# Kernel tuning notes

Hardware: AMD Instinct MI355X
Metric: run time of the kernel (lower is better)

## Reference

```python
import jax, jax.numpy as jnp
import numpy as np

N = 100000    # nodes
E = 800000    # directed edges
EF = 16       # edge features
NF = 1        # node features (forced by the module's MLP-size constraint)
HID = NF * 8  # NNConv out = 8
H1, C1 = 8, 16  # gat1 heads / per-head channels -> 128
NC = 16       # num_classes (gat2: heads=1, out=NC)


def setup_inputs() -> dict:
    key = jax.random.key(0)
    ks = jax.random.split(key, 20)
    s = 0.1
    return {
        "x": jax.random.normal(ks[0], (N, NF), jnp.float32),
        "edge_index": jax.random.randint(ks[1], (2, E), 0, N, jnp.int64),
        "edge_attr": jax.random.normal(ks[2], (E, EF), jnp.float32),
        # edge MLP: Linear(EF,8) -> ReLU -> Linear(8,8)
        "w1": jax.random.normal(ks[3], (EF, HID), jnp.float32) * s,
        "b1": jnp.zeros((HID,), jnp.float32),
        "w2": jax.random.normal(ks[4], (HID, HID), jnp.float32) * s,
        "b2": jnp.zeros((HID,), jnp.float32),
        # NNConv root weight + bias
        "root": jax.random.normal(ks[5], (NF, HID), jnp.float32) * s,
        "nn_bias": jnp.zeros((HID,), jnp.float32),
        # GAT1: in 8 -> 16 ch x 8 heads
        "g1W": jax.random.normal(ks[6], (HID, H1 * C1), jnp.float32) * s,
        "g1as": jax.random.normal(ks[7], (H1, C1), jnp.float32) * s,
        "g1ad": jax.random.normal(ks[8], (H1, C1), jnp.float32) * s,
        "g1b": jnp.zeros((H1 * C1,), jnp.float32),
        # GAT2: in 128 -> NC, 1 head
        "g2W": jax.random.normal(ks[9], (H1 * C1, NC), jnp.float32) * s,
        "g2as": jax.random.normal(ks[10], (1, NC), jnp.float32) * s,
        "g2ad": jax.random.normal(ks[11], (1, NC), jnp.float32) * s,
        "g2b": jnp.zeros((NC,), jnp.float32),
    }


def _gat(h_in, W, a_src, a_dst, bias, src, dst, n, heads, ch):
    # h: [N, heads, ch]
    h = (h_in @ W).reshape(n, heads, ch)
    e_s = jnp.einsum("nhc,hc->nh", h, a_src)   # per-node src logits
    e_d = jnp.einsum("nhc,hc->nh", h, a_dst)
    e = jax.nn.leaky_relu(e_s[src] + e_d[dst], 0.2)      # [E2, heads]
    m = jax.ops.segment_max(e, dst, num_segments=n)      # segment softmax
    e = jnp.exp(e - m[dst])
    z = jax.ops.segment_sum(e, dst, num_segments=n)
    alpha = e / (z[dst] + 1e-16)                          # [E2, heads]
    out = jax.ops.segment_sum(alpha[:, :, None] * h[src], dst, num_segments=n)
    return out.reshape(n, heads * ch) + bias


def reference(x, edge_index, edge_attr, w1, b1, w2, b2, root, nn_bias,
              g1W, g1as, g1ad, g1b, g2W, g2as, g2ad, g2b):
    n = x.shape[0]
    src, dst = edge_index[0], edge_index[1]

    # ---- NNConv (aggr='mean'): per-edge weight from edge MLP ----
    w_e = jax.nn.relu(edge_attr @ w1 + b1) @ w2 + b2      # [E, NF*HID]
    w_e = w_e.reshape(-1, NF, HID)
    msg = jnp.einsum("ei,eio->eo", x[src], w_e)            # [E, HID]
    sums = jax.ops.segment_sum(msg, dst, num_segments=n)
    cnt = jax.ops.segment_sum(jnp.ones((msg.shape[0],), msg.dtype), dst, num_segments=n)
    aggr = sums / jnp.maximum(cnt, 1.0)[:, None]
    h = jax.nn.relu(aggr + x @ root + nn_bias)             # [N, 8]
    # dropout: eval mode -> identity

    # ---- add self-loops (PyG GATConv default) ----
    loops = jnp.arange(n, dtype=src.dtype)
    src2 = jnp.concatenate([src, loops])
    dst2 = jnp.concatenate([dst, loops])

    h = jax.nn.elu(_gat(h, g1W, g1as, g1ad, g1b, src2, dst2, n, H1, C1))  # [N,128]
    out = _gat(h, g2W, g2as, g2ad, g2b, src2, dst2, n, 1, NC)             # [N,16]
    return jax.nn.log_softmax(out, axis=1)
```

## Files before the change

### kernel.cpp

```cpp
#include <hip/hip_runtime.h>
#include <hip/hip_fp16.h>
#include <math.h>

constexpr int NN  = 100000;
constexpr int NE  = 800000;
constexpr int H1 = 8, C1 = 16;
constexpr int D1 = H1 * C1;
constexpr int NC = 16;
constexpr int CAP = 40;
constexpr float LOG2E = 1.44269504f;

static inline int cdiv(int a, int b) { return (a + b - 1) / b; }

typedef int   v4i __attribute__((ext_vector_type(4)));
typedef float v2f __attribute__((ext_vector_type(2)));

__device__ inline __half2 h2_bits(unsigned u) {
    __half2 r; __builtin_memcpy(&r, &u, 4); return r;
}
__device__ inline __half2 shflx_h2(__half2 v, int off) {
    int iv; __builtin_memcpy(&iv, &v, 4);
    iv = __shfl_xor(iv, off);
    __half2 r; __builtin_memcpy(&r, &iv, 4); return r;
}

__global__ void fill_cur(int* __restrict__ cur) {
    int i = blockIdx.x * blockDim.x + threadIdx.x;
    if (i < NN) cur[i] = i * CAP;
}

__global__ void nnconv_scatter(const float* __restrict__ x,
                               const int* __restrict__ src, const int* __restrict__ dst,
                               const float* __restrict__ ea,
                               const float* __restrict__ w1, const float* __restrict__ b1,
                               const float* __restrict__ w2, const float* __restrict__ b2,
                               int* __restrict__ cursor,
                               int* __restrict__ src_s, __half* __restrict__ msg_s) {
    __shared__ float sw1[16 * 8], sw2[8 * 8], sb1[8], sb2[8];
    int t = threadIdx.x;
    if (t < 128) sw1[t] = w1[t];
    else if (t < 192) sw2[t - 128] = w2[t - 128];
    else if (t < 200) sb1[t - 192] = b1[t - 192];
    else if (t < 208) sb2[t - 200] = b2[t - 200];
    __syncthreads();
    int e = blockIdx.x * blockDim.x + t;
    if (e >= NE) return;

    float a[16];
    const float4* ea4 = (const float4*)(ea + (size_t)e * 16);
    float4 v0 = ea4[0], v1 = ea4[1], v2 = ea4[2], v3 = ea4[3];
    a[0]=v0.x; a[1]=v0.y; a[2]=v0.z; a[3]=v0.w;
    a[4]=v1.x; a[5]=v1.y; a[6]=v1.z; a[7]=v1.w;
    a[8]=v2.x; a[9]=v2.y; a[10]=v2.z; a[11]=v2.w;
    a[12]=v3.x; a[13]=v3.y; a[14]=v3.z; a[15]=v3.w;

    float hdn[8];
#pragma unroll
    for (int j = 0; j < 8; j++) {
        float s = sb1[j];
#pragma unroll
        for (int i = 0; i < 16; i++) s = fmaf(a[i], sw1[i * 8 + j], s);
        hdn[j] = fmaxf(s, 0.f);
    }
    int sn = src[e], dn = dst[e];
    float xv = x[sn];
    __align__(16) __half msg[8];
#pragma unroll
    for (int j = 0; j < 8; j++) {
        float s = sb2[j];
#pragma unroll
        for (int i = 0; i < 8; i++) s = fmaf(hdn[i], sw2[i * 8 + j], s);
        msg[j] = __float2half(xv * s);
    }
    int pos = atomicAdd(&cursor[dn], 1);
    if (pos < dn * CAP + CAP) {
        v4i mv; __builtin_memcpy(&mv, msg, 16);
        __builtin_nontemporal_store(mv, (v4i*)(msg_s + (unsigned)pos * 8u));
        src_s[pos] = sn;
    }
}

__global__ void fused_node1(const float* __restrict__ x,
                            const int* __restrict__ cur,
                            const __half* __restrict__ msg_s,
                            const float* __restrict__ root, const float* __restrict__ nb,
                            const float* __restrict__ W,
                            const float* __restrict__ as_, const float* __restrict__ ad_,
                            unsigned char* __restrict__ h1f8,
                            float* __restrict__ es, float* __restrict__ ed) {
    int t = blockIdx.x * blockDim.x + threadIdx.x;
    if (t >= NN * 8) return;
    int n = t >> 3, j = t & 7;
    int rs = n * CAP;
    int d = min(cur[n] - rs, CAP);

    float p0 = 0.f, p1 = 0.f, p2 = 0.f, p3 = 0.f;
    float p4 = 0.f, p5 = 0.f, p6 = 0.f, p7 = 0.f;
    for (int k = j; k < d; k += 8) {
        uint4 m = *(const uint4*)(msg_s + (unsigned)(rs + k) * 8u);
        float2 f0 = __half22float2(h2_bits(m.x));
        float2 f1 = __half22float2(h2_bits(m.y));
        float2 f2 = __half22float2(h2_bits(m.z));
        float2 f3 = __half22float2(h2_bits(m.w));
        p0 += f0.x; p1 += f0.y; p2 += f1.x; p3 += f1.y;
        p4 += f2.x; p5 += f2.y; p6 += f3.x; p7 += f3.y;
    }
    float k0 = (j & 4) ? p4 : p0, s0 = (j & 4) ? p0 : p4;
    float k1 = (j & 4) ? p5 : p1, s1 = (j & 4) ? p1 : p5;
    float k2 = (j & 4) ? p6 : p2, s2 = (j & 4) ? p2 : p6;
    float k3 = (j & 4) ? p7 : p3, s3 = (j & 4) ? p3 : p7;
    k0 += __shfl_xor(s0, 4); k1 += __shfl_xor(s1, 4);
    k2 += __shfl_xor(s2, 4); k3 += __shfl_xor(s3, 4);
    float m0 = (j & 2) ? k2 : k0, n0 = (j & 2) ? k0 : k2;
    float m1 = (j & 2) ? k3 : k1, n1 = (j & 2) ? k1 : k3;
    m0 += __shfl_xor(n0, 2); m1 += __shfl_xor(n1, 2);
    float q  = (j & 1) ? m1 : m0, r = (j & 1) ? m0 : m1;
    float sum = q + __shfl_xor(r, 1);

    float hj = fmaxf(sum / fmaxf((float)d, 1.f) + x[n] * root[j] + nb[j], 0.f);

    float hv[8];
#pragma unroll
    for (int k = 0; k < 8; k++) hv[k] = __shfl(hj, k, 8);

    int hd = j;
    float acc[16];
#pragma unroll
    for (int c = 0; c < 16; c++) acc[c] = 0.f;
#pragma unroll
    for (int k = 0; k < 8; k++) {
        const float* wr = W + k * D1 + hd * 16;
#pragma unroll
        for (int c = 0; c < 16; c++) acc[c] = fmaf(hv[k], wr[c], acc[c]);
    }
    float s = 0.f, dd = 0.f;
#pragma unroll
    for (int c = 0; c < 16; c++) {
        s = fmaf(acc[c], as_[hd * 16 + c], s);
        dd = fmaf(acc[c], ad_[hd * 16 + c], dd);
    }
    v4i pk;
#pragma unroll
    for (int w = 0; w < 4; w++) {
        int wd = __builtin_amdgcn_cvt_pk_fp8_f32(acc[4*w] * 16.f, acc[4*w+1] * 16.f, 0, false);
        wd = __builtin_amdgcn_cvt_pk_fp8_f32(acc[4*w+2] * 16.f, acc[4*w+3] * 16.f, wd, true);
        pk[w] = wd;
    }
    *(v4i*)(h1f8 + (unsigned)n * 128u + hd * 16) = pk;
    es[t] = s * LOG2E;
    ed[t] = dd * LOG2E;
}

__global__ __launch_bounds__(256) void gat1_gather(
        const int* __restrict__ cur,
        const int* __restrict__ src_s,
        const float* __restrict__ es, const float* __restrict__ ed,
        const unsigned char* __restrict__ h1f8, const float* __restrict__ b,
        const float* __restrict__ W2,
        const float* __restrict__ as2, const float* __restrict__ ad2,
        __half* __restrict__ h2h, float* __restrict__ es2, float* __restrict__ ed2) {
    __shared__ float sW2[2048];
    __shared__ float so[4][4][132];
    int tid = threadIdx.x;
    for (int idx = tid; idx < 2048; idx += 256) sW2[idx] = W2[idx];
    __syncthreads();

    int wv = tid >> 6, lane = tid & 63;
    int g  = lane >> 4;
    int cl = lane & 15;
    int hd = cl >> 1;
    float4 bv0 = *((const float4*)(b + cl * 8));
    float4 bv1 = *((const float4*)(b + cl * 8 + 4));

    int base = (blockIdx.x * 4 + wv) * 4;
    for (int i = 0; i < 4; i++) {
        int node = base + i;
        int rs = node * CAP;
        int d = min(cur[node] - rs, CAP);
        const int* sp = src_s + rs;
        float edn = ed[(unsigned)node * 8u + hd];

        float vs = es[(unsigned)node * 8u + hd] + edn;
        vs = fmaxf(vs, 0.2f * vs);
        float a0 = (g == 0) ? __builtin_amdgcn_exp2f(vs) : 0.f;
        float z = a0;
        uint2 gl = *(const uint2*)(h1f8 + (unsigned)node * 128u + cl * 8);
        v2f d0 = __builtin_amdgcn_cvt_pk_f32_fp8(gl.x, false);
        v2f d1 = __builtin_amdgcn_cvt_pk_f32_fp8(gl.x, true);
        v2f d2 = __builtin_amdgcn_cvt_pk_f32_fp8(gl.y, false);
        v2f d3 = __builtin_amdgcn_cvt_pk_f32_fp8(gl.y, true);
        float c0 = a0 * d0[0], c1 = a0 * d0[1], c2 = a0 * d1[0], c3 = a0 * d1[1];
        float c4 = a0 * d2[0], c5 = a0 * d2[1], c6 = a0 * d3[0], c7 = a0 * d3[1];

        for (int k = g; k < d; k += 4) {
            int s = sp[k];
            float v = es[(unsigned)s * 8u + hd] + edn;
            v = fmaxf(v, 0.2f * v);
            float a = __builtin_amdgcn_exp2f(v);
            uint2 ge = *(const uint2*)(h1f8 + (unsigned)s * 128u + cl * 8);
            v2f e0 = __builtin_amdgcn_cvt_pk_f32_fp8(ge.x, false);
            v2f e1 = __builtin_amdgcn_cvt_pk_f32_fp8(ge.x, true);
            v2f e2 = __builtin_amdgcn_cvt_pk_f32_fp8(ge.y, false);
            v2f e3 = __builtin_amdgcn_cvt_pk_f32_fp8(ge.y, true);
            z += a;
            c0 = fmaf(a, e0[0], c0); c1 = fmaf(a, e0[1], c1);
            c2 = fmaf(a, e1[0], c2); c3 = fmaf(a, e1[1], c3);
            c4 = fmaf(a, e2[0], c4); c5 = fmaf(a, e2[1], c5);
            c6 = fmaf(a, e3[0], c6); c7 = fmaf(a, e3[1], c7);
        }
        z += __shfl_xor(z, 16); z += __shfl_xor(z, 32);
        c0 += __shfl_xor(c0, 16); c0 += __shfl_xor(c0, 32);
        c1 += __shfl_xor(c1, 16); c1 += __shfl_xor(c1, 32);
        c2 += __shfl_xor(c2, 16); c2 += __shfl_xor(c2, 32);
        c3 += __shfl_xor(c3, 16); c3 += __shfl_xor(c3, 32);
        c4 += __shfl_xor(c4, 16); c4 += __shfl_xor(c4, 32);
        c5 += __shfl_xor(c5, 16); c5 += __shfl_xor(c5, 32);
        c6 += __shfl_xor(c6, 16); c6 += __shfl_xor(c6, 32);
        c7 += __shfl_xor(c7, 16); c7 += __shfl_xor(c7, 32);

        float rz = 1.f / (16.f * (z + 1e-16f));
        float o0 = fmaf(c0, rz, bv0.x), o1 = fmaf(c1, rz, bv0.y);
        float o2 = fmaf(c2, rz, bv0.z), o3 = fmaf(c3, rz, bv0.w);
        float o4 = fmaf(c4, rz, bv1.x), o5 = fmaf(c5, rz, bv1.y);
        float o6 = fmaf(c6, rz, bv1.z), o7 = fmaf(c7, rz, bv1.w);
        o0 = o0 > 0.f ? o0 : __expf(o0) - 1.f;
        o1 = o1 > 0.f ? o1 : __expf(o1) - 1.f;
        o2 = o2 > 0.f ? o2 : __expf(o2) - 1.f;
        o3 = o3 > 0.f ? o3 : __expf(o3) - 1.f;
        o4 = o4 > 0.f ? o4 : __expf(o4) - 1.f;
        o5 = o5 > 0.f ? o5 : __expf(o5) - 1.f;
        o6 = o6 > 0.f ? o6 : __expf(o6) - 1.f;
        o7 = o7 > 0.f ? o7 : __expf(o7) - 1.f;
        if (g == 0) {
            float4* sp2 = (float4*)&so[wv][i][cl * 8];
            sp2[0] = make_float4(o0, o1, o2, o3);
            sp2[1] = make_float4(o4, o5, o6, o7);
        }
    }
    __asm__ __volatile__("s_waitcnt lgkmcnt(0)" ::: "memory");

    int nl = lane >> 4, c = lane & 15;
    float partial = 0.f;
#pragma unroll 4
    for (int k = 0; k < 128; k += 2) {
        float2 sv = *(const float2*)&so[wv][nl][k];
        partial = fmaf(sv.x, sW2[k * 16 + c], partial);
        partial = fmaf(sv.y, sW2[(k + 1) * 16 + c], partial);
    }
    float ta = partial * as2[c], tb = partial * ad2[c];
#pragma unroll
    for (int off = 1; off < 16; off <<= 1) {
        ta += __shfl_xor(ta, off);
        tb += __shfl_xor(tb, off);
    }
    h2h[(unsigned)(base + nl) * 16u + c] = __float2half(partial);
    if (c == 0) {
        es2[base + nl] = ta * LOG2E;
        ed2[base + nl] = tb * LOG2E;
    }
}

__global__ __launch_bounds__(256) void gat2_gather(
        const int* __restrict__ cur,
        const int* __restrict__ src_s,
        const float* __restrict__ es, const float* __restrict__ ed,
        const __half* __restrict__ h2h, const float* __restrict__ b,
        float* __restrict__ out) {
    int tid = threadIdx.x;
    int wv = tid >> 6, lane = tid & 63;
    int g = lane >> 3, l = lane & 7;
    const unsigned* h2i = (const unsigned*)h2h;
    float2 bv = ((const float2*)b)[l];
    int base = (blockIdx.x * 4 + wv) * 4;
    for (int i = 0; i < 4; i++) {
        int node = base + i;
        int rs = node * CAP;
        int d = min(cur[node] - rs, CAP);
        const int* sp = src_s + rs;
        float edn = ed[node];
        float vs = es[node] + edn;
        vs = fmaxf(vs, 0.2f * vs);
        float a0 = (g == 0) ? __builtin_amdgcn_exp2f(vs) : 0.f;
        float z = a0;
        __half2 acc = __hmul2(__float2half2_rn(a0),
                              h2_bits(h2i[(unsigned)node * 8u + l]));

        for (int k = g; k < d; k += 8) {
            int s = sp[k];
            float v = es[s] + edn;
            v = fmaxf(v, 0.2f * v);
            float a = __builtin_amdgcn_exp2f(v);
            unsigned hraw = h2i[(unsigned)s * 8u + l];
            z += a;
            acc = __hfma2(__float2half2_rn(a), h2_bits(hraw), acc);
        }
        z += __shfl_xor(z, 8); z += __shfl_xor(z, 16); z += __shfl_xor(z, 32);
        acc = __hadd2(acc, shflx_h2(acc, 8));
        acc = __hadd2(acc, shflx_h2(acc, 16));
        acc = __hadd2(acc, shflx_h2(acc, 32));

        float rz = 1.f / (z + 1e-16f);
        float2 f = __half22float2(acc);
        float o0 = fmaf(f.x, rz, bv.x);
        float o1 = fmaf(f.y, rz, bv.y);
        float mx = fmaxf(o0, o1);
        mx = fmaxf(mx, __shfl_xor(mx, 1));
        mx = fmaxf(mx, __shfl_xor(mx, 2));
        mx = fmaxf(mx, __shfl_xor(mx, 4));
        float ss = __expf(o0 - mx) + __expf(o1 - mx);
        ss += __shfl_xor(ss, 1); ss += __shfl_xor(ss, 2); ss += __shfl_xor(ss, 4);
        float lg = mx + __logf(ss);
        if (g == 0)
            ((float2*)out)[(unsigned)node * 8u + l] = make_float2(o0 - lg, o1 - lg);
    }
}

extern "C" void kernel_launch(void* const* d_in, const int* in_sizes, int n_in,
                              void* d_out, int out_size, void* d_ws, size_t ws_size,
                              hipStream_t stream) {
    const float* x    = (const float*)d_in[0];
    const int*   ei   = (const int*)d_in[1];
    const float* ea   = (const float*)d_in[2];
    const float* w1   = (const float*)d_in[3];
    const float* b1   = (const float*)d_in[4];
    const float* w2   = (const float*)d_in[5];
    const float* b2   = (const float*)d_in[6];
    const float* root = (const float*)d_in[7];
    const float* nb   = (const float*)d_in[8];
    const float* g1W  = (const float*)d_in[9];
    const float* g1as = (const float*)d_in[10];
    const float* g1ad = (const float*)d_in[11];
    const float* g1b  = (const float*)d_in[12];
    const float* g2W  = (const float*)d_in[13];
    const float* g2as = (const float*)d_in[14];
    const float* g2ad = (const float*)d_in[15];
    const float* g2b  = (const float*)d_in[16];
    float* out = (float*)d_out;

    const int* src = ei;
    const int* dst = ei + NE;

    float* ws = (float*)d_ws;
    size_t o = 0;
    __half* msg_s  = (__half*)(ws + o); o += (size_t)NN * CAP * 4;
    unsigned char* h1f8 = (unsigned char*)(ws + o); o += (size_t)NN * 32;
    __half* h2h    = (__half*)(ws + o); o += (size_t)NN * NC / 2;
    int*  src_s = (int*)(ws + o); o += (size_t)NN * CAP;
    int*  cur   = (int*)(ws + o); o += NN;
    float* es1  = ws + o; o += (size_t)NN * H1;
    float* ed1  = ws + o; o += (size_t)NN * H1;
    float* es2  = ws + o; o += NN;
    float* ed2  = ws + o; o += NN;
    (void)ws_size; (void)in_sizes; (void)n_in; (void)out_size;

    const int B = 256;

    fill_cur<<<cdiv(NN, B), B, 0, stream>>>(cur);

    nnconv_scatter<<<cdiv(NE, B), B, 0, stream>>>(x, src, dst, ea, w1, b1, w2, b2,
                                                  cur, src_s, msg_s);
    fused_node1<<<cdiv(NN * 8, B), B, 0, stream>>>(x, cur, msg_s, root, nb,
                                                   g1W, g1as, g1ad, h1f8, es1, ed1);
    gat1_gather<<<NN / 16, B, 0, stream>>>(cur, src_s, es1, ed1, h1f8,
                                           g1b, g2W, g2as, g2ad, h2h, es2, ed2);
    gat2_gather<<<NN / 16, B, 0, stream>>>(cur, src_s, es2, ed2, h2h, g2b, out);
}
```

Measured before the change: 299.3 us.

## Move edge MLP from scatter into node aggregation, store (src, edge id) slots

The scatter kernel now only builds the per-destination slot list, storing source index and edge id as an int2 and no longer computing or writing fp16 messages. The node kernel reads each slot, gathers the edge attributes by edge id, recomputes the edge MLP message in fp32 and sums it. This removes the msg_s write and reread and the fp16 rounding of messages, but swaps a sequential streaming read of edge_attr for a random 64-byte gather per edge. The GAT kernels now read source indices with stride 2, which uses more bandwidth on those index loads.

```diff
diff --git a/kernel.cpp b/kernel.cpp
--- a/kernel.cpp
+++ b/kernel.cpp
@@ -29,66 +29,38 @@
     if (i < NN) cur[i] = i * CAP;
 }
 
-__global__ void nnconv_scatter(const float* __restrict__ x,
-                               const int* __restrict__ src, const int* __restrict__ dst,
-                               const float* __restrict__ ea,
-                               const float* __restrict__ w1, const float* __restrict__ b1,
-                               const float* __restrict__ w2, const float* __restrict__ b2,
-                               int* __restrict__ cursor,
-                               int* __restrict__ src_s, __half* __restrict__ msg_s) {
-    __shared__ float sw1[16 * 8], sw2[8 * 8], sb1[8], sb2[8];
-    int t = threadIdx.x;
-    if (t < 128) sw1[t] = w1[t];
-    else if (t < 192) sw2[t - 128] = w2[t - 128];
-    else if (t < 200) sb1[t - 192] = b1[t - 192];
-    else if (t < 208) sb2[t - 200] = b2[t - 200];
-    __syncthreads();
-    int e = blockIdx.x * blockDim.x + t;
+__global__ void scatter_csr(const int* __restrict__ src, const int* __restrict__ dst,
+                            int* __restrict__ cursor, int* __restrict__ slots) {
+    int e = blockIdx.x * blockDim.x + threadIdx.x;
     if (e >= NE) return;
-
-    float a[16];
-    const float4* ea4 = (const float4*)(ea + (size_t)e * 16);
-    float4 v0 = ea4[0], v1 = ea4[1], v2 = ea4[2], v3 = ea4[3];
-    a[0]=v0.x; a[1]=v0.y; a[2]=v0.z; a[3]=v0.w;
-    a[4]=v1.x; a[5]=v1.y; a[6]=v1.z; a[7]=v1.w;
-    a[8]=v2.x; a[9]=v2.y; a[10]=v2.z; a[11]=v2.w;
-    a[12]=v3.x; a[13]=v3.y; a[14]=v3.z; a[15]=v3.w;
-
-    float hdn[8];
-#pragma unroll
-    for (int j = 0; j < 8; j++) {
-        float s = sb1[j];
-#pragma unroll
-        for (int i = 0; i < 16; i++) s = fmaf(a[i], sw1[i * 8 + j], s);
-        hdn[j] = fmaxf(s, 0.f);
-    }
     int sn = src[e], dn = dst[e];
-    float xv = x[sn];
-    __align__(16) __half msg[8];
-#pragma unroll
-    for (int j = 0; j < 8; j++) {
-        float s = sb2[j];
-#pragma unroll
-        for (int i = 0; i < 8; i++) s = fmaf(hdn[i], sw2[i * 8 + j], s);
-        msg[j] = __float2half(xv * s);
-    }
     int pos = atomicAdd(&cursor[dn], 1);
     if (pos < dn * CAP + CAP) {
-        v4i mv; __builtin_memcpy(&mv, msg, 16);
-        __builtin_nontemporal_store(mv, (v4i*)(msg_s + (unsigned)pos * 8u));
-        src_s[pos] = sn;
+        int2 v; v.x = sn; v.y = e;
+        *(int2*)(slots + (size_t)pos * 2) = v;
     }
 }
 
 __global__ void fused_node1(const float* __restrict__ x,
                             const int* __restrict__ cur,
-                            const __half* __restrict__ msg_s,
+                            const int* __restrict__ slots,
+                            const float* __restrict__ ea,
+                            const float* __restrict__ w1, const float* __restrict__ b1,
+                            const float* __restrict__ w2, const float* __restrict__ b2,
                             const float* __restrict__ root, const float* __restrict__ nb,
                             const float* __restrict__ W,
                             const float* __restrict__ as_, const float* __restrict__ ad_,
                             unsigned char* __restrict__ h1f8,
                             float* __restrict__ es, float* __restrict__ ed) {
-    int t = blockIdx.x * blockDim.x + threadIdx.x;
+    __shared__ float sw1[16 * 8], sw2[8 * 8], sb1[8], sb2[8];
+    int tl = threadIdx.x;
+    if (tl < 128) sw1[tl] = w1[tl];
+    else if (tl < 192) sw2[tl - 128] = w2[tl - 128];
+    else if (tl < 200) sb1[tl - 192] = b1[tl - 192];
+    else if (tl < 208) sb2[tl - 200] = b2[tl - 200];
+    __syncthreads();
+
+    int t = blockIdx.x * blockDim.x + tl;
     if (t >= NN * 8) return;
     int n = t >> 3, j = t & 7;
     int rs = n * CAP;
@@ -97,13 +69,34 @@
     float p0 = 0.f, p1 = 0.f, p2 = 0.f, p3 = 0.f;
     float p4 = 0.f, p5 = 0.f, p6 = 0.f, p7 = 0.f;
     for (int k = j; k < d; k += 8) {
-        uint4 m = *(const uint4*)(msg_s + (unsigned)(rs + k) * 8u);
-        float2 f0 = __half22float2(h2_bits(m.x));
-        float2 f1 = __half22float2(h2_bits(m.y));
-        float2 f2 = __half22float2(h2_bits(m.z));
-        float2 f3 = __half22float2(h2_bits(m.w));
-        p0 += f0.x; p1 += f0.y; p2 += f1.x; p3 += f1.y;
-        p4 += f2.x; p5 += f2.y; p6 += f3.x; p7 += f3.y;
+        int2 se = *(const int2*)(slots + (size_t)(rs + k) * 2);
+        int sn = se.x, eid = se.y;
+        float xv = x[sn];
+        const float4* ea4 = (const float4*)(ea + (size_t)eid * 16);
+        float4 v0 = ea4[0], v1 = ea4[1], v2 = ea4[2], v3 = ea4[3];
+        float a[16];
+        a[0]=v0.x; a[1]=v0.y; a[2]=v0.z; a[3]=v0.w;
+        a[4]=v1.x; a[5]=v1.y; a[6]=v1.z; a[7]=v1.w;
+        a[8]=v2.x; a[9]=v2.y; a[10]=v2.z; a[11]=v2.w;
+        a[12]=v3.x; a[13]=v3.y; a[14]=v3.z; a[15]=v3.w;
+        float hdn[8];
+#pragma unroll
+        for (int c = 0; c < 8; c++) {
+            float s = sb1[c];
+#pragma unroll
+            for (int i = 0; i < 16; i++) s = fmaf(a[i], sw1[i * 8 + c], s);
+            hdn[c] = fmaxf(s, 0.f);
+        }
+        float m[8];
+#pragma unroll
+        for (int c = 0; c < 8; c++) {
+            float s = sb2[c];
+#pragma unroll
+            for (int i = 0; i < 8; i++) s = fmaf(hdn[i], sw2[i * 8 + c], s);
+            m[c] = xv * s;
+        }
+        p0 += m[0]; p1 += m[1]; p2 += m[2]; p3 += m[3];
+        p4 += m[4]; p5 += m[5]; p6 += m[6]; p7 += m[7];
     }
     float k0 = (j & 4) ? p4 : p0, s0 = (j & 4) ? p0 : p4;
     float k1 = (j & 4) ? p5 : p1, s1 = (j & 4) ? p1 : p5;
@@ -153,7 +146,7 @@
 
 __global__ __launch_bounds__(256) void gat1_gather(
         const int* __restrict__ cur,
-        const int* __restrict__ src_s,
+        const int* __restrict__ slots,
         const float* __restrict__ es, const float* __restrict__ ed,
         const unsigned char* __restrict__ h1f8, const float* __restrict__ b,
         const float* __restrict__ W2,
@@ -177,7 +170,7 @@
         int node = base + i;
         int rs = node * CAP;
         int d = min(cur[node] - rs, CAP);
-        const int* sp = src_s + rs;
+        const int* sp = slots + (size_t)rs * 2;
         float edn = ed[(unsigned)node * 8u + hd];
 
         float vs = es[(unsigned)node * 8u + hd] + edn;
@@ -193,7 +186,7 @@
         float c4 = a0 * d2[0], c5 = a0 * d2[1], c6 = a0 * d3[0], c7 = a0 * d3[1];
 
         for (int k = g; k < d; k += 4) {
-            int s = sp[k];
+            int s = sp[k << 1];
             float v = es[(unsigned)s * 8u + hd] + edn;
             v = fmaxf(v, 0.2f * v);
             float a = __builtin_amdgcn_exp2f(v);
@@ -262,7 +255,7 @@
 
 __global__ __launch_bounds__(256) void gat2_gather(
         const int* __restrict__ cur,
-        const int* __restrict__ src_s,
+        const int* __restrict__ slots,
         const float* __restrict__ es, const float* __restrict__ ed,
         const __half* __restrict__ h2h, const float* __restrict__ b,
         float* __restrict__ out) {
@@ -276,7 +269,7 @@
         int node = base + i;
         int rs = node * CAP;
         int d = min(cur[node] - rs, CAP);
-        const int* sp = src_s + rs;
+        const int* sp = slots + (size_t)rs * 2;
         float edn = ed[node];
         float vs = es[node] + edn;
         vs = fmaxf(vs, 0.2f * vs);
@@ -286,7 +279,7 @@
                               h2_bits(h2i[(unsigned)node * 8u + l]));
 
         for (int k = g; k < d; k += 8) {
-            int s = sp[k];
+            int s = sp[k << 1];
             float v = es[s] + edn;
             v = fmaxf(v, 0.2f * v);
             float a = __builtin_amdgcn_exp2f(v);
@@ -342,10 +335,9 @@
 
     float* ws = (float*)d_ws;
     size_t o = 0;
-    __half* msg_s  = (__half*)(ws + o); o += (size_t)NN * CAP * 4;
+    int* slots = (int*)(ws + o); o += (size_t)NN * CAP * 2;
     unsigned char* h1f8 = (unsigned char*)(ws + o); o += (size_t)NN * 32;
     __half* h2h    = (__half*)(ws + o); o += (size_t)NN * NC / 2;
-    int*  src_s = (int*)(ws + o); o += (size_t)NN * CAP;
     int*  cur   = (int*)(ws + o); o += NN;
     float* es1  = ws + o; o += (size_t)NN * H1;
     float* ed1  = ws + o; o += (size_t)NN * H1;
@@ -357,11 +349,11 @@
 
     fill_cur<<<cdiv(NN, B), B, 0, stream>>>(cur);
 
-    nnconv_scatter<<<cdiv(NE, B), B, 0, stream>>>(x, src, dst, ea, w1, b1, w2, b2,
-                                                  cur, src_s, msg_s);
-    fused_node1<<<cdiv(NN * 8, B), B, 0, stream>>>(x, cur, msg_s, root, nb,
-                                                   g1W, g1as, g1ad, h1f8, es1, ed1);
-    gat1_gather<<<NN / 16, B, 0, stream>>>(cur, src_s, es1, ed1, h1f8,
+    scatter_csr<<<cdiv(NE, B), B, 0, stream>>>(src, dst, cur, slots);
+    fused_node1<<<cdiv(NN * 8, B), B, 0, stream>>>(x, cur, slots, ea, w1, b1, w2, b2,
+                                                   root, nb, g1W, g1as, g1ad,
+                                                   h1f8, es1, ed1);
+    gat1_gather<<<NN / 16, B, 0, stream>>>(cur, slots, es1, ed1, h1f8,
                                            g1b, g2W, g2as, g2ad, h2h, es2, ed2);
-    gat2_gather<<<NN / 16, B, 0, stream>>>(cur, src_s, es2, ed2, h2h, g2b, out);
-}
+    gat2_gather<<<NN / 16, B, 0, stream>>>(cur, slots, es2, ed2, h2h, g2b, out);
+}
```

Measured after the change: 531.9 us. 77.7% more time.

## Pack source index and FP8 NNConv message into one 16-byte edge record

Applied to the files above, without the earlier changes.

The scatter kernel now writes a single interleaved 16-byte record per edge, holding the source index and the eight messages quantized to FP8 with a scale of 32. Before, it wrote a separate half-precision message array plus a separate source-index array. The point is one store per edge instead of two, which cuts the scattered memory transactions in the atomic-placement pass. The cost is that the GAT gather kernels now read source indices at a 16-byte stride, which wastes bandwidth on those reads. FP8 messages also lose precision relative to fp16.

```diff
diff --git a/kernel.cpp b/kernel.cpp
--- a/kernel.cpp
+++ b/kernel.cpp
@@ -9,6 +9,7 @@
 constexpr int NC = 16;
 constexpr int CAP = 40;
 constexpr float LOG2E = 1.44269504f;
+constexpr float MSC   = 32.f;
 
 static inline int cdiv(int a, int b) { return (a + b - 1) / b; }
 
@@ -35,7 +36,7 @@
                                const float* __restrict__ w1, const float* __restrict__ b1,
                                const float* __restrict__ w2, const float* __restrict__ b2,
                                int* __restrict__ cursor,
-                               int* __restrict__ src_s, __half* __restrict__ msg_s) {
+                               int* __restrict__ rec_s) {
     __shared__ float sw1[16 * 8], sw2[8 * 8], sb1[8], sb2[8];
     int t = threadIdx.x;
     if (t < 128) sw1[t] = w1[t];
@@ -63,26 +64,30 @@
         hdn[j] = fmaxf(s, 0.f);
     }
     int sn = src[e], dn = dst[e];
-    float xv = x[sn];
-    __align__(16) __half msg[8];
+    float xv = x[sn] * MSC;
+    float m[8];
 #pragma unroll
     for (int j = 0; j < 8; j++) {
         float s = sb2[j];
 #pragma unroll
         for (int i = 0; i < 8; i++) s = fmaf(hdn[i], sw2[i * 8 + j], s);
-        msg[j] = __float2half(xv * s);
-    }
+        m[j] = xv * s;
+    }
+    int wa = __builtin_amdgcn_cvt_pk_fp8_f32(m[0], m[1], 0, false);
+    wa     = __builtin_amdgcn_cvt_pk_fp8_f32(m[2], m[3], wa, true);
+    int wb = __builtin_amdgcn_cvt_pk_fp8_f32(m[4], m[5], 0, false);
+    wb     = __builtin_amdgcn_cvt_pk_fp8_f32(m[6], m[7], wb, true);
+
     int pos = atomicAdd(&cursor[dn], 1);
     if (pos < dn * CAP + CAP) {
-        v4i mv; __builtin_memcpy(&mv, msg, 16);
-        __builtin_nontemporal_store(mv, (v4i*)(msg_s + (unsigned)pos * 8u));
-        src_s[pos] = sn;
+        v4i rec; rec[0] = sn; rec[1] = wa; rec[2] = wb; rec[3] = 0;
+        __builtin_nontemporal_store(rec, (v4i*)(rec_s + (size_t)pos * 4));
     }
 }
 
 __global__ void fused_node1(const float* __restrict__ x,
                             const int* __restrict__ cur,
-                            const __half* __restrict__ msg_s,
+                            const int* __restrict__ rec_s,
                             const float* __restrict__ root, const float* __restrict__ nb,
                             const float* __restrict__ W,
                             const float* __restrict__ as_, const float* __restrict__ ad_,
@@ -97,13 +102,13 @@
     float p0 = 0.f, p1 = 0.f, p2 = 0.f, p3 = 0.f;
     float p4 = 0.f, p5 = 0.f, p6 = 0.f, p7 = 0.f;
     for (int k = j; k < d; k += 8) {
-        uint4 m = *(const uint4*)(msg_s + (unsigned)(rs + k) * 8u);
-        float2 f0 = __half22float2(h2_bits(m.x));
-        float2 f1 = __half22float2(h2_bits(m.y));
-        float2 f2 = __half22float2(h2_bits(m.z));
-        float2 f3 = __half22float2(h2_bits(m.w));
-        p0 += f0.x; p1 += f0.y; p2 += f1.x; p3 += f1.y;
-        p4 += f2.x; p5 += f2.y; p6 += f3.x; p7 += f3.y;
+        uint4 m = *(const uint4*)(rec_s + (size_t)(rs + k) * 4);
+        v2f f0 = __builtin_amdgcn_cvt_pk_f32_fp8(m.y, false);
+        v2f f1 = __builtin_amdgcn_cvt_pk_f32_fp8(m.y, true);
+        v2f f2 = __builtin_amdgcn_cvt_pk_f32_fp8(m.z, false);
+        v2f f3 = __builtin_amdgcn_cvt_pk_f32_fp8(m.z, true);
+        p0 += f0[0]; p1 += f0[1]; p2 += f1[0]; p3 += f1[1];
+        p4 += f2[0]; p5 += f2[1]; p6 += f3[0]; p7 += f3[1];
     }
     float k0 = (j & 4) ? p4 : p0, s0 = (j & 4) ? p0 : p4;
     float k1 = (j & 4) ? p5 : p1, s1 = (j & 4) ? p1 : p5;
@@ -117,7 +122,8 @@
     float q  = (j & 1) ? m1 : m0, r = (j & 1) ? m0 : m1;
     float sum = q + __shfl_xor(r, 1);
 
-    float hj = fmaxf(sum / fmaxf((float)d, 1.f) + x[n] * root[j] + nb[j], 0.f);
+    float inv = 1.f / (MSC * fmaxf((float)d, 1.f));
+    float hj = fmaxf(fmaf(sum, inv, x[n] * root[j] + nb[j]), 0.f);
 
     float hv[8];
 #pragma unroll
@@ -153,7 +159,7 @@
 
 __global__ __launch_bounds__(256) void gat1_gather(
         const int* __restrict__ cur,
-        const int* __restrict__ src_s,
+        const int* __restrict__ rec_s,
         const float* __restrict__ es, const float* __restrict__ ed,
         const unsigned char* __restrict__ h1f8, const float* __restrict__ b,
         const float* __restrict__ W2,
@@ -177,7 +183,7 @@
         int node = base + i;
         int rs = node * CAP;
         int d = min(cur[node] - rs, CAP);
-        const int* sp = src_s + rs;
+        const int* sp = rec_s + (size_t)rs * 4;
         float edn = ed[(unsigned)node * 8u + hd];
 
         float vs = es[(unsigned)node * 8u + hd] + edn;
@@ -193,7 +199,7 @@
         float c4 = a0 * d2[0], c5 = a0 * d2[1], c6 = a0 * d3[0], c7 = a0 * d3[1];
 
         for (int k = g; k < d; k += 4) {
-            int s = sp[k];
+            int s = sp[k << 2];
             float v = es[(unsigned)s * 8u + hd] + edn;
             v = fmaxf(v, 0.2f * v);
             float a = __builtin_amdgcn_exp2f(v);
@@ -262,7 +268,7 @@
 
 __global__ __launch_bounds__(256) void gat2_gather(
         const int* __restrict__ cur,
-        const int* __restrict__ src_s,
+        const int* __restrict__ rec_s,
         const float* __restrict__ es, const float* __restrict__ ed,
         const __half* __restrict__ h2h, const float* __restrict__ b,
         float* __restrict__ out) {
@@ -276,7 +282,7 @@
         int node = base + i;
         int rs = node * CAP;
         int d = min(cur[node] - rs, CAP);
-        const int* sp = src_s + rs;
+        const int* sp = rec_s + (size_t)rs * 4;
         float edn = ed[node];
         float vs = es[node] + edn;
         vs = fmaxf(vs, 0.2f * vs);
@@ -286,7 +292,7 @@
                               h2_bits(h2i[(unsigned)node * 8u + l]));
 
         for (int k = g; k < d; k += 8) {
-            int s = sp[k];
+            int s = sp[k << 2];
             float v = es[s] + edn;
             v = fmaxf(v, 0.2f * v);
             float a = __builtin_amdgcn_exp2f(v);
@@ -342,10 +348,9 @@
 
     float* ws = (float*)d_ws;
     size_t o = 0;
-    __half* msg_s  = (__half*)(ws + o); o += (size_t)NN * CAP * 4;
+    int* rec_s = (int*)(ws + o); o += (size_t)NN * CAP * 4;
     unsigned char* h1f8 = (unsigned char*)(ws + o); o += (size_t)NN * 32;
     __half* h2h    = (__half*)(ws + o); o += (size_t)NN * NC / 2;
-    int*  src_s = (int*)(ws + o); o += (size_t)NN * CAP;
     int*  cur   = (int*)(ws + o); o += NN;
     float* es1  = ws + o; o += (size_t)NN * H1;
     float* ed1  = ws + o; o += (size_t)NN * H1;
@@ -358,10 +363,10 @@
     fill_cur<<<cdiv(NN, B), B, 0, stream>>>(cur);
 
     nnconv_scatter<<<cdiv(NE, B), B, 0, stream>>>(x, src, dst, ea, w1, b1, w2, b2,
-                                                  cur, src_s, msg_s);
-    fused_node1<<<cdiv(NN * 8, B), B, 0, stream>>>(x, cur, msg_s, root, nb,
+                                                  cur, rec_s);
+    fused_node1<<<cdiv(NN * 8, B), B, 0, stream>>>(x, cur, rec_s, root, nb,
                                                    g1W, g1as, g1ad, h1f8, es1, ed1);
-    gat1_gather<<<NN / 16, B, 0, stream>>>(cur, src_s, es1, ed1, h1f8,
+    gat1_gather<<<NN / 16, B, 0, stream>>>(cur, rec_s, es1, ed1, h1f8,
                                            g1b, g2W, g2as, g2ad, h2h, es2, ed2);
-    gat2_gather<<<NN / 16, B, 0, stream>>>(cur, src_s, es2, ed2, h2h, g2b, out);
-}
+    gat2_gather<<<NN / 16, B, 0, stream>>>(cur, rec_s, es2, ed2, h2h, g2b, out);
+}
```

After: 297.3 us. No clear change (-0.7%).
